# Optimization experiments

Hardware: AMD Instinct MI355X
Metric: run time of the kernel (lower is better)

Reference implementation:

```python
import jax, jax.numpy as jnp
import numpy as np

N, T, I, H = 256, 256, 512, 512

def setup_inputs() -> dict:
    key = jax.random.key(0)
    ks = jax.random.split(key, 9)
    s = 1.0 / np.sqrt(H)  # torch GRUCell init scale
    x = jax.random.normal(ks[0], (N, T, I), jnp.float32)
    is_init = jax.random.bernoulli(ks[1], 0.05, (N, T))  # bool resets
    hx = jax.random.normal(ks[2], (N, T, H), jnp.float32)
    W_ih = jax.random.uniform(ks[3], (3 * H, I), jnp.float32, -s, s)
    W_hh = jax.random.uniform(ks[4], (3 * H, H), jnp.float32, -s, s)
    b_ih = jax.random.uniform(ks[5], (3 * H,), jnp.float32, -s, s)
    b_hh = jax.random.uniform(ks[6], (3 * H,), jnp.float32, -s, s)
    W_out = jax.random.uniform(ks[7], (H, H), jnp.float32, -s, s)
    b_out = jax.random.uniform(ks[8], (H,), jnp.float32, -s, s)
    return {"x": x, "hx": hx, "W_ih": W_ih, "W_hh": W_hh, "b_ih": b_ih,
            "b_hh": b_hh, "W_out": W_out, "b_out": b_out, "is_init": is_init}

def _gru_forward(x, hx, W_ih, W_hh, b_ih, b_hh, W_out, b_out, is_init):
    # recurrent_mode branch; learnable_init=False -> reset to zeros
    mask = is_init[..., None]                         # [N,T,1] bool
    h0 = jnp.where(mask[:, 0], 0.0, hx[:, 0])        # [N,H]
    # precompute input-to-hidden gates for all steps: [N,T,3H]
    xi = jnp.einsum('nti,gi->ntg', x, W_ih) + b_ih

    def step(h, inp):
        xi_t, m_t = inp                              # [N,3H], [N,1]
        h = jnp.where(m_t, 0.0, h)                   # per-step init masking
        hh = h @ W_hh.T + b_hh                       # [N,3H]
        xr, xz, xn = jnp.split(xi_t, 3, axis=-1)
        hr, hz, hn = jnp.split(hh, 3, axis=-1)
        r = jax.nn.sigmoid(xr + hr)
        z = jax.nn.sigmoid(xz + hz)
        n = jnp.tanh(xn + r * hn)
        h_new = (1.0 - z) * n + z * h
        return h_new, h_new

    hT, hs = jax.lax.scan(step, h0,
                          (xi.transpose(1, 0, 2), mask.transpose(1, 0, 2)))
    hs = hs.transpose(1, 0, 2)                       # [N,T,H]
    output = hs @ W_out.T + b_out                    # LazyLinear projection
    hx_out = jnp.broadcast_to(hT[:, None, :], (hT.shape[0], T, hT.shape[1]))
    return output, hx_out

def reference(x, hx, W_ih, W_hh, b_ih, b_hh, W_out, b_out, is_init):
    return _gru_forward(x, hx, W_ih, W_hh, b_ih, b_hh, W_out, b_out, is_init)
```

## Files before the change

kernel.cpp:

```cpp
#include <hip/hip_runtime.h>

#define NB 256
#define TT 256
#define II 512
#define HH 512
#define GG 1536

typedef unsigned short ushort_t;
typedef unsigned int uint_t;
typedef unsigned long long ull_t;
typedef __attribute__((ext_vector_type(8))) short short8;
typedef __attribute__((ext_vector_type(4))) float f32x4;

typedef __attribute__((address_space(3))) void lds_void;
typedef const __attribute__((address_space(1))) void glb_void;

__device__ __forceinline__ ushort_t f2bf(float f) {
  union { float f; unsigned int u; } x; x.f = f;
  unsigned int r = x.u + 0x7FFFu + ((x.u >> 16) & 1u);
  return (ushort_t)(r >> 16);
}
__device__ __forceinline__ float bf2f(ushort_t b) {
  union { unsigned int u; float f; } x; x.u = ((unsigned int)b) << 16;
  return x.f;
}
__device__ __forceinline__ float sigmoidf_(float x) {
  return __fdividef(1.0f, 1.0f + __expf(-x));
}
__device__ __forceinline__ float tanhf_(float x) {
  float t = __expf(2.0f * x);
  return 1.0f - __fdividef(2.0f, t + 1.0f);
}
__device__ __forceinline__ short8 pack8(float4 a, float4 b) {
  short8 r;
  r[0] = (short)f2bf(a.x); r[1] = (short)f2bf(a.y);
  r[2] = (short)f2bf(a.z); r[3] = (short)f2bf(a.w);
  r[4] = (short)f2bf(b.x); r[5] = (short)f2bf(b.y);
  r[6] = (short)f2bf(b.z); r[7] = (short)f2bf(b.w);
  return r;
}

__global__ void mask_detect_kernel(const unsigned char* __restrict__ src,
                                   unsigned char* __restrict__ mask8) {
  __shared__ int fByte, fOdd;
  const int tid = threadIdx.x;
  if (tid == 0) { fByte = 0; fOdd = 0; }
  __syncthreads();
  const uint_t* w = (const uint_t*)src;
  int ab = 0, ao = 0;
  for (int i = tid; i < NB * TT; i += blockDim.x) {
    if ((i & 3) == 1 && src[i]) ab = 1;
    if (i < 16384 && (i & 1) == 1 && w[i]) ao = 1;
  }
  if (ab) fByte = 1;
  if (ao) fOdd = 1;
  __syncthreads();
  const int isByte = fByte, isW32 = fOdd;
  for (int i = tid; i < NB * TT; i += blockDim.x) {
    unsigned char m;
    if (isByte)      m = src[i] ? 1 : 0;
    else if (isW32)  m = w[i] ? 1 : 0;
    else             m = w[2 * i] ? 1 : 0;
    mask8[i] = m;
  }
}

__global__ void cvt_f2bf(const float* __restrict__ src, ushort_t* __restrict__ dst,
                         int n4) {
  int stride = gridDim.x * blockDim.x;
  for (int i = blockIdx.x * blockDim.x + threadIdx.x; i < n4; i += stride) {
    const float4 v = reinterpret_cast<const float4*>(src)[i];
    ushort4 o;
    o.x = f2bf(v.x); o.y = f2bf(v.y); o.z = f2bf(v.z); o.w = f2bf(v.w);
    reinterpret_cast<ushort4*>(dst)[i] = o;
  }
}

__global__ void pack_whh(const float* __restrict__ W, ushort_t* __restrict__ out) {
  int idx = blockIdx.x * blockDim.x + threadIdx.x;
  if (idx >= 96 * 16 * 64) return;
  int l = idx & 63;
  int tk = idx >> 6;
  int tile = tk >> 4, kk = tk & 15;
  int row = tile * 16 + (l & 15);
  int k = kk * 32 + (l >> 4) * 8;
  const float* s = W + (size_t)row * HH + k;
  short8 v;
#pragma unroll
  for (int e = 0; e < 8; ++e) v[e] = (short)f2bf(s[e]);
  *reinterpret_cast<short8*>(out + (size_t)idx * 8) = v;
}

template <int AF32, int CF32>
__global__ __launch_bounds__(256) void gemm_bt(
    const void* __restrict__ Av, const ushort_t* __restrict__ B,
    const float* __restrict__ bias, void* __restrict__ Cv, int NC) {
  __shared__ ushort_t As[128 * 32];
  __shared__ ushort_t Bs[128 * 32];
  const int tid = threadIdx.x;
  const int lane = tid & 63;
  const int w = tid >> 6;
  const int wr = w >> 1, wc = w & 1;
  const int c15 = lane & 15, l4 = lane >> 4;
  const int mbase = blockIdx.x * 128;
  const int nbase = blockIdx.y * 128;

  const int rs = tid >> 2;
  const int kb = (tid & 3) * 8;

  f32x4 acc[4][4] = {};

  const float4* Bg = reinterpret_cast<const float4*>(B);
  auto bIdx = [&](int c, int kt) {
    return ((size_t)(nbase + rs + 64 * c) * 512 + kt * 32 + kb) >> 3;
  };
  float4 rb0 = Bg[bIdx(0, 0)], rb1 = Bg[bIdx(1, 0)];

  const float4* Agf = reinterpret_cast<const float4*>(Av);
  auto aEl = [&](int c, int kt) {
    return (size_t)(mbase + rs + 64 * c) * 512 + kt * 32 + kb;
  };
  float4 a0a, a0b, a1a, a1b;
  float4 h0, h1;
  if constexpr (AF32) {
    a0a = Agf[aEl(0, 0) >> 2]; a0b = Agf[(aEl(0, 0) >> 2) + 1];
    a1a = Agf[aEl(1, 0) >> 2]; a1b = Agf[(aEl(1, 0) >> 2) + 1];
  } else {
    h0 = Agf[aEl(0, 0) >> 3];
    h1 = Agf[aEl(1, 0) >> 3];
  }

  for (int kt = 0; kt < 16; ++kt) {
    __syncthreads();
    if constexpr (AF32) {
      *reinterpret_cast<short8*>(&As[(size_t)tid * 8]) = pack8(a0a, a0b);
      *reinterpret_cast<short8*>(&As[(size_t)(tid + 256) * 8]) = pack8(a1a, a1b);
    } else {
      reinterpret_cast<float4*>(As)[tid] = h0;
      reinterpret_cast<float4*>(As)[tid + 256] = h1;
    }
    reinterpret_cast<float4*>(Bs)[tid] = rb0;
    reinterpret_cast<float4*>(Bs)[tid + 256] = rb1;
    if (kt < 15) {
      if constexpr (AF32) {
        a0a = Agf[aEl(0, kt + 1) >> 2]; a0b = Agf[(aEl(0, kt + 1) >> 2) + 1];
        a1a = Agf[aEl(1, kt + 1) >> 2]; a1b = Agf[(aEl(1, kt + 1) >> 2) + 1];
      } else {
        h0 = Agf[aEl(0, kt + 1) >> 3];
        h1 = Agf[aEl(1, kt + 1) >> 3];
      }
      rb0 = Bg[bIdx(0, kt + 1)]; rb1 = Bg[bIdx(1, kt + 1)];
    }
    __syncthreads();
    short8 af[4], bq[4];
#pragma unroll
    for (int m = 0; m < 4; ++m)
      af[m] = *reinterpret_cast<const short8*>(&As[(wr * 64 + m * 16 + c15) * 32 + l4 * 8]);
#pragma unroll
    for (int n = 0; n < 4; ++n)
      bq[n] = *reinterpret_cast<const short8*>(&Bs[(wc * 64 + n * 16 + c15) * 32 + l4 * 8]);
#pragma unroll
    for (int m = 0; m < 4; ++m)
#pragma unroll
      for (int n = 0; n < 4; ++n)
        acc[m][n] = __builtin_amdgcn_mfma_f32_16x16x32_bf16(af[m], bq[n], acc[m][n], 0, 0, 0);
  }

#pragma unroll
  for (int n = 0; n < 4; ++n) {
    const int col = nbase + wc * 64 + n * 16 + c15;
    const float bv = bias[col];
#pragma unroll
    for (int m = 0; m < 4; ++m) {
      const int row = mbase + wr * 64 + m * 16 + l4 * 4;
#pragma unroll
      for (int q = 0; q < 4; ++q) {
        const float v = acc[m][n][q] + bv;
        if constexpr (CF32)
          reinterpret_cast<float*>(Cv)[(size_t)(row + q) * NC + col] = v;
        else
          reinterpret_cast<ushort_t*>(Cv)[(size_t)(row + q) * NC + col] = f2bf(v);
      }
    }
  }
}

__global__ __launch_bounds__(256, 1) void gru_rec(
    const ushort_t* __restrict__ xi, const ushort_t* __restrict__ Wpk,
    const float* __restrict__ hx, const float* __restrict__ bhh,
    const unsigned char* __restrict__ mask8,
    ushort_t* __restrict__ hs, float* __restrict__ hT,
    char* __restrict__ xch) {
  extern __shared__ ushort_t smem[];
  const int HAF_U = 65536, XIL_U = 73728, HST_U = 79872;

  const int tid = threadIdx.x;
  const int lane = tid & 63;
  const int w = tid >> 6;
  const int c15 = lane & 15, l4 = lane >> 4;
  const int bid = blockIdx.x;
  const int a = bid & 7;
  const int b = bid >> 3;
  const int n0 = b * 16;

  const int jl = w * 16 + c15;
  const int jfull = a * 64 + jl;
  const float br = bhh[jfull], bz = bhh[512 + jfull], bn = bhh[1024 + jfull];

#pragma unroll
  for (int g = 0; g < 2; ++g)
#pragma unroll
    for (int kk = 0; kk < 16; ++kk)
      __builtin_amdgcn_global_load_lds(
          (glb_void*)(Wpk + ((size_t)((g * 32 + a * 4 + w) * 16 + kk)) * 512 + lane * 8),
          (lds_void*)(smem + w * 16384 + (g * 16 + kk) * 512 + lane * 8), 16, 0, 0);

  const int wb2 = ((2 * 32 + a * 4 + w) * 16) * 512 + lane * 8;
  short8 wn[16];
#pragma unroll
  for (int kk = 0; kk < 16; ++kk)
    wn[kk] = *(const short8*)(Wpk + wb2 + kk * 512);

  size_t xg0, xg1 = 0;
  {
    int c = tid, s = c / 24, r = c % 24, g = r >> 3, p = r & 7;
    xg0 = ((size_t)(n0 + s) * TT) * GG + g * 512 + a * 64 + p * 8;
    if (tid < 128) {
      c = tid + 256; s = c / 24; r = c % 24; g = r >> 3; p = r & 7;
      xg1 = ((size_t)(n0 + s) * TT) * GG + g * 512 + a * 64 + p * 8;
    }
  }
  const int xl0 = tid * 8, xl1 = (tid + 256) * 8;

  char* slot0 = xch + (size_t)(b * 2) * 32768;
  char* slot1 = xch + (size_t)(b * 2 + 1) * 32768;

  const int ps = tid >> 4, pj = tid & 15;
  const int pOff = (2 * a + (pj >> 3)) * 1024 +
                   (ps + 16 * ((pj >> 1) & 3)) * 16 + (pj & 1) * 8;
  const int pSrc = HST_U + ps * 72 + pj * 4;

  auto publish = [&](char* slot, uint_t tag) {
    const uint_t h0 = smem[pSrc], h1 = smem[pSrc + 1];
    const uint_t h2 = smem[pSrc + 2], h3 = smem[pSrc + 3];
    const ull_t w0 = ((ull_t)(h0 << 16 | tag)) | (((ull_t)(h1 << 16 | tag)) << 32);
    const ull_t w1 = ((ull_t)(h2 << 16 | tag)) | (((ull_t)(h3 << 16 | tag)) << 32);
    char* d = slot + (size_t)pOff * 2;
    __hip_atomic_store((ull_t*)d, w0, __ATOMIC_RELAXED, __HIP_MEMORY_SCOPE_AGENT);
    __hip_atomic_store((ull_t*)(d + 8), w1, __ATOMIC_RELAXED, __HIP_MEMORY_SCOPE_AGENT);
  };

  float h[4];
#pragma unroll
  for (int q = 0; q < 4; ++q) {
    const int s = l4 * 4 + q;
    const bool mk0 = mask8[(size_t)(n0 + s) * TT] != 0;
    const float v = mk0 ? 0.0f : hx[((size_t)(n0 + s) * TT) * HH + jfull];
    h[q] = v;
    smem[HST_U + s * 72 + jl] = f2bf(v);
  }
  __syncthreads();
  publish(slot0, 1u);

  for (int t = 0; t < TT; ++t) {
    ushort_t* xb = smem + XIL_U + (t & 1) * 3072;
    __builtin_amdgcn_global_load_lds((glb_void*)(xi + xg0 + (size_t)t * GG),
                                     (lds_void*)(xb + xl0), 16, 0, 0);
    if (tid < 128)
      __builtin_amdgcn_global_load_lds((glb_void*)(xi + xg1 + (size_t)t * GG),
                                       (lds_void*)(xb + xl1), 16, 0, 0);

    const char* src = (t & 1) ? slot1 : slot0;
    const uint_t tgt = (uint_t)(t + 1);
    ull_t v[16];
    bool ok;
    do {
      ok = true;
#pragma unroll
      for (int i = 0; i < 16; ++i)
        v[i] = __hip_atomic_load((const ull_t*)(src + ((size_t)(tid + i * 256)) * 8),
                                 __ATOMIC_RELAXED, __HIP_MEMORY_SCOPE_AGENT);
#pragma unroll
      for (int i = 0; i < 16; ++i)
        ok &= (((uint_t)v[i] & 0xFFFFu) == tgt) &&
              (((uint_t)(v[i] >> 32) & 0xFFFFu) == tgt);
    } while (!ok);
#pragma unroll
    for (int i = 0; i < 16; ++i) {
      const uint_t lo = (uint_t)(v[i] >> 16) & 0xFFFFu;
      const uint_t hi = (uint_t)(v[i] >> 48);
      *(uint_t*)((char*)smem + HAF_U * 2 + ((size_t)(tid + i * 256)) * 4) =
          lo | (hi << 16);
    }

    const bool domask = (t + 1 < TT);
    const int tn = domask ? (t + 1) : t;
    unsigned char mkv[4];
#pragma unroll
    for (int q = 0; q < 4; ++q)
      mkv[q] = mask8[(size_t)(n0 + l4 * 4 + q) * TT + tn];

    __syncthreads();

    short8 af[16];
#pragma unroll
    for (int kk = 0; kk < 16; ++kk)
      af[kk] = *(const short8*)((char*)smem + HAF_U * 2 + kk * 1024 + lane * 16);

    f32x4 a0 = {0.f, 0.f, 0.f, 0.f}, a1 = a0, a2 = a0;
#pragma unroll
    for (int kk = 0; kk < 16; ++kk) {
      const short8 w0 = *(const short8*)(smem + w * 16384 + kk * 512 + lane * 8);
      const short8 w1 = *(const short8*)(smem + w * 16384 + (16 + kk) * 512 + lane * 8);
      a0 = __builtin_amdgcn_mfma_f32_16x16x32_bf16(af[kk], w0, a0, 0, 0, 0);
      a1 = __builtin_amdgcn_mfma_f32_16x16x32_bf16(af[kk], w1, a1, 0, 0, 0);
      a2 = __builtin_amdgcn_mfma_f32_16x16x32_bf16(af[kk], wn[kk], a2, 0, 0, 0);
    }

#pragma unroll
    for (int q = 0; q < 4; ++q) {
      const int s = l4 * 4 + q;
      const float xr = bf2f(xb[s * 192 + jl]);
      const float xz = bf2f(xb[s * 192 + 64 + jl]);
      const float xn = bf2f(xb[s * 192 + 128 + jl]);
      const float rr = sigmoidf_(xr + a0[q] + br);
      const float zz = sigmoidf_(xz + a1[q] + bz);
      const float nn = tanhf_(xn + rr * (a2[q] + bn));
      const float hnew = (1.0f - zz) * nn + zz * h[q];
      __builtin_nontemporal_store(
          f2bf(hnew), &hs[((size_t)(n0 + s) * TT + t) * HH + jfull]);
      const float hp = (domask && mkv[q]) ? 0.0f : hnew;
      h[q] = hp;
      smem[HST_U + s * 72 + jl] = f2bf(hp);
    }
    __syncthreads();

    if (domask)
      publish(((t + 1) & 1) ? slot1 : slot0, (uint_t)(t + 2));
  }

#pragma unroll
  for (int q = 0; q < 4; ++q)
    hT[(size_t)(n0 + l4 * 4 + q) * HH + jfull] = h[q];
}

__global__ void bcast_hT(const float* __restrict__ hT, float* __restrict__ dst) {
  const float4* s = (const float4*)hT;
  float4* d = (float4*)dst;
  const int total = NB * TT * HH / 4;
  const int stride = gridDim.x * blockDim.x;
  for (int c = blockIdx.x * blockDim.x + threadIdx.x; c < total; c += stride) {
    int n = c >> 15;
    int j4 = c & 127;
    d[c] = s[(n << 7) | j4];
  }
}

extern "C" void kernel_launch(void* const* d_in, const int* in_sizes, int n_in,
                              void* d_out, int out_size, void* d_ws, size_t ws_size,
                              hipStream_t stream) {
  const float* x    = (const float*)d_in[0];
  const float* hx   = (const float*)d_in[1];
  const float* Wih  = (const float*)d_in[2];
  const float* Whh  = (const float*)d_in[3];
  const float* bih  = (const float*)d_in[4];
  const float* bhh  = (const float*)d_in[5];
  const float* Wout = (const float*)d_in[6];
  const float* bout = (const float*)d_in[7];
  const unsigned char* isinit = (const unsigned char*)d_in[8];

  char* ws = (char*)d_ws;
  ushort_t* xi    = (ushort_t*)(ws);
  ushort_t* wihb  = (ushort_t*)(ws + 201326592);
  ushort_t* whhp  = (ushort_t*)(ws + 202899456);
  ushort_t* woutb = (ushort_t*)(ws + 204472320);
  unsigned char* mask8 = (unsigned char*)(ws + 204996608);
  float*    hTbuf = (float*)(ws + 205062144);
  char*     xch   = (char*)(ws + 205602816);

  float* out1 = (float*)d_out;
  float* out2 = out1 + (size_t)NB * TT * HH;
  ushort_t* hsb = (ushort_t*)out2;

  hipMemsetAsync(xch, 0, 1 << 20, stream);
  mask_detect_kernel<<<1, 1024, 0, stream>>>(isinit, mask8);
  cvt_f2bf<<<768, 256, 0, stream>>>(Wih, wihb, GG * II / 4);
  cvt_f2bf<<<256, 256, 0, stream>>>(Wout, woutb, HH * HH / 4);
  pack_whh<<<384, 256, 0, stream>>>(Whh, whhp);

  dim3 g1(512, 12);
  gemm_bt<1, 0><<<g1, 256, 0, stream>>>((const void*)x, wihb, bih, (void*)xi, GG);

  gru_rec<<<128, 256, 162048, stream>>>(xi, whhp, hx, bhh, mask8, hsb, hTbuf,
                                        xch);

  dim3 g3(512, 4);
  gemm_bt<0, 1><<<g3, 256, 0, stream>>>((const void*)hsb, woutb, bout, (void*)out1, HH);

  bcast_hT<<<2048, 256, 0, stream>>>(hTbuf, out2);
}
```

Baseline: 1.349 ms.

## Publish hidden state directly from registers and skip polling own slice

The recurrent GRU kernel now has each lane pair shuffle its new bf16 hidden values and write them straight into a double-buffered LDS A-fragment and the global exchange slot. This removes the staging buffer and the second per-step __syncthreads. Each block no longer polls or copies its own slice of the exchange buffer. The r-gate weights move from LDS into registers alongside the n-gate weights, which shrinks LDS but adds register pressure. The hs stores are deferred until after publishing, so the cross-block critical path is shorter.

```diff
diff --git a/kernel.cpp b/kernel.cpp
--- a/kernel.cpp
+++ b/kernel.cpp
@@ -192,7 +192,7 @@
     ushort_t* __restrict__ hs, float* __restrict__ hT,
     char* __restrict__ xch) {
   extern __shared__ ushort_t smem[];
-  const int HAF_U = 65536, XIL_U = 73728, HST_U = 79872;
+  const int HAF_U = 32768, XIL_U = 49152;
 
   const int tid = threadIdx.x;
   const int lane = tid & 63;
@@ -208,18 +208,19 @@
   const float br = bhh[jfull], bz = bhh[512 + jfull], bn = bhh[1024 + jfull];
 
 #pragma unroll
-  for (int g = 0; g < 2; ++g)
-#pragma unroll
-    for (int kk = 0; kk < 16; ++kk)
-      __builtin_amdgcn_global_load_lds(
-          (glb_void*)(Wpk + ((size_t)((g * 32 + a * 4 + w) * 16 + kk)) * 512 + lane * 8),
-          (lds_void*)(smem + w * 16384 + (g * 16 + kk) * 512 + lane * 8), 16, 0, 0);
-
-  const int wb2 = ((2 * 32 + a * 4 + w) * 16) * 512 + lane * 8;
-  short8 wn[16];
-#pragma unroll
   for (int kk = 0; kk < 16; ++kk)
-    wn[kk] = *(const short8*)(Wpk + wb2 + kk * 512);
+    __builtin_amdgcn_global_load_lds(
+        (glb_void*)(Wpk + ((size_t)((32 + a * 4 + w) * 16 + kk)) * 512 + lane * 8),
+        (lds_void*)(smem + w * 8192 + kk * 512 + lane * 8), 16, 0, 0);
+
+  const int wbr = ((0 * 32 + a * 4 + w) * 16) * 512 + lane * 8;
+  const int wbn = ((2 * 32 + a * 4 + w) * 16) * 512 + lane * 8;
+  short8 wr_[16], wn_[16];
+#pragma unroll
+  for (int kk = 0; kk < 16; ++kk) {
+    wr_[kk] = *(const short8*)(Wpk + wbr + kk * 512);
+    wn_[kk] = *(const short8*)(Wpk + wbn + kk * 512);
+  }
 
   size_t xg0, xg1 = 0;
   {
@@ -235,32 +236,44 @@
   char* slot0 = xch + (size_t)(b * 2) * 32768;
   char* slot1 = xch + (size_t)(b * 2 + 1) * 32768;
 
-  const int ps = tid >> 4, pj = tid & 15;
-  const int pOff = (2 * a + (pj >> 3)) * 1024 +
-                   (ps + 16 * ((pj >> 1) & 3)) * 16 + (pj & 1) * 8;
-  const int pSrc = HST_U + ps * 72 + pj * 4;
-
-  auto publish = [&](char* slot, uint_t tag) {
-    const uint_t h0 = smem[pSrc], h1 = smem[pSrc + 1];
-    const uint_t h2 = smem[pSrc + 2], h3 = smem[pSrc + 3];
-    const ull_t w0 = ((ull_t)(h0 << 16 | tag)) | (((ull_t)(h1 << 16 | tag)) << 32);
-    const ull_t w1 = ((ull_t)(h2 << 16 | tag)) | (((ull_t)(h3 << 16 | tag)) << 32);
-    char* d = slot + (size_t)pOff * 2;
-    __hip_atomic_store((ull_t*)d, w0, __ATOMIC_RELAXED, __HIP_MEMORY_SCOPE_AGENT);
-    __hip_atomic_store((ull_t*)(d + 8), w1, __ATOMIC_RELAXED, __HIP_MEMORY_SCOPE_AGENT);
+  const bool evenlane = ((c15 & 1) == 0);
+  auto ubOff = [&](int s, int j) {
+    return (j >> 5) * 1024 + (s + 16 * ((j & 31) >> 3)) * 16 + (j & 7) * 2;
   };
 
+  auto pubfill = [&](char* slot, uint_t tag, int pp, const ushort_t* hb) {
+    const uint_t u01 = (uint_t)hb[0] | ((uint_t)hb[1] << 16);
+    const uint_t u23 = (uint_t)hb[2] | ((uint_t)hb[3] << 16);
+    const uint_t p01 = __shfl_xor(u01, 1);
+    const uint_t p23 = __shfl_xor(u23, 1);
+    if (evenlane) {
+      char* hafB = (char*)(smem + HAF_U + pp * 8192);
+#pragma unroll
+      for (int q = 0; q < 4; ++q) {
+        const int s = l4 * 4 + q;
+        const uint_t own = ((q < 2 ? u01 : u23) >> ((q & 1) * 16)) & 0xFFFFu;
+        const uint_t prt = ((q < 2 ? p01 : p23) >> ((q & 1) * 16)) & 0xFFFFu;
+        const int ub = ubOff(s, jfull);
+        *(uint_t*)(hafB + ub) = own | (prt << 16);
+        const ull_t wv = ((ull_t)((own << 16) | tag)) |
+                         (((ull_t)((prt << 16) | tag)) << 32);
+        __hip_atomic_store((ull_t*)(slot + (size_t)ub * 2), wv,
+                           __ATOMIC_RELAXED, __HIP_MEMORY_SCOPE_AGENT);
+      }
+    }
+  };
+
   float h[4];
+  ushort_t hb0[4];
 #pragma unroll
   for (int q = 0; q < 4; ++q) {
     const int s = l4 * 4 + q;
     const bool mk0 = mask8[(size_t)(n0 + s) * TT] != 0;
     const float v = mk0 ? 0.0f : hx[((size_t)(n0 + s) * TT) * HH + jfull];
     h[q] = v;
-    smem[HST_U + s * 72 + jl] = f2bf(v);
-  }
-  __syncthreads();
-  publish(slot0, 1u);
+    hb0[q] = f2bf(v);
+  }
+  pubfill(slot0, 1u, 0, hb0);
 
   for (int t = 0; t < TT; ++t) {
     ushort_t* xb = smem + XIL_U + (t & 1) * 3072;
@@ -282,16 +295,18 @@
                                  __ATOMIC_RELAXED, __HIP_MEMORY_SCOPE_AGENT);
 #pragma unroll
       for (int i = 0; i < 16; ++i)
-        ok &= (((uint_t)v[i] & 0xFFFFu) == tgt) &&
-              (((uint_t)(v[i] >> 32) & 0xFFFFu) == tgt);
+        if ((i >> 1) != a)
+          ok &= (((uint_t)v[i] & 0xFFFFu) == tgt) &&
+                (((uint_t)(v[i] >> 32) & 0xFFFFu) == tgt);
     } while (!ok);
-#pragma unroll
-    for (int i = 0; i < 16; ++i) {
-      const uint_t lo = (uint_t)(v[i] >> 16) & 0xFFFFu;
-      const uint_t hi = (uint_t)(v[i] >> 48);
-      *(uint_t*)((char*)smem + HAF_U * 2 + ((size_t)(tid + i * 256)) * 4) =
-          lo | (hi << 16);
-    }
+    char* hafB = (char*)(smem + HAF_U + (t & 1) * 8192);
+#pragma unroll
+    for (int i = 0; i < 16; ++i)
+      if ((i >> 1) != a) {
+        const uint_t lo = (uint_t)(v[i] >> 16) & 0xFFFFu;
+        const uint_t hi = (uint_t)(v[i] >> 48);
+        *(uint_t*)(hafB + ((size_t)(tid + i * 256)) * 4) = lo | (hi << 16);
+      }
 
     const bool domask = (t + 1 < TT);
     const int tn = domask ? (t + 1) : t;
@@ -305,18 +320,18 @@
     short8 af[16];
 #pragma unroll
     for (int kk = 0; kk < 16; ++kk)
-      af[kk] = *(const short8*)((char*)smem + HAF_U * 2 + kk * 1024 + lane * 16);
+      af[kk] = *(const short8*)(hafB + kk * 1024 + lane * 16);
 
     f32x4 a0 = {0.f, 0.f, 0.f, 0.f}, a1 = a0, a2 = a0;
 #pragma unroll
     for (int kk = 0; kk < 16; ++kk) {
-      const short8 w0 = *(const short8*)(smem + w * 16384 + kk * 512 + lane * 8);
-      const short8 w1 = *(const short8*)(smem + w * 16384 + (16 + kk) * 512 + lane * 8);
-      a0 = __builtin_amdgcn_mfma_f32_16x16x32_bf16(af[kk], w0, a0, 0, 0, 0);
-      a1 = __builtin_amdgcn_mfma_f32_16x16x32_bf16(af[kk], w1, a1, 0, 0, 0);
-      a2 = __builtin_amdgcn_mfma_f32_16x16x32_bf16(af[kk], wn[kk], a2, 0, 0, 0);
-    }
-
+      const short8 wz = *(const short8*)(smem + w * 8192 + kk * 512 + lane * 8);
+      a0 = __builtin_amdgcn_mfma_f32_16x16x32_bf16(af[kk], wr_[kk], a0, 0, 0, 0);
+      a1 = __builtin_amdgcn_mfma_f32_16x16x32_bf16(af[kk], wz, a1, 0, 0, 0);
+      a2 = __builtin_amdgcn_mfma_f32_16x16x32_bf16(af[kk], wn_[kk], a2, 0, 0, 0);
+    }
+
+    ushort_t hbp[4], hsv[4];
 #pragma unroll
     for (int q = 0; q < 4; ++q) {
       const int s = l4 * 4 + q;
@@ -327,16 +342,17 @@
       const float zz = sigmoidf_(xz + a1[q] + bz);
       const float nn = tanhf_(xn + rr * (a2[q] + bn));
       const float hnew = (1.0f - zz) * nn + zz * h[q];
-      __builtin_nontemporal_store(
-          f2bf(hnew), &hs[((size_t)(n0 + s) * TT + t) * HH + jfull]);
+      hsv[q] = f2bf(hnew);
       const float hp = (domask && mkv[q]) ? 0.0f : hnew;
       h[q] = hp;
-      smem[HST_U + s * 72 + jl] = f2bf(hp);
-    }
-    __syncthreads();
-
+      hbp[q] = f2bf(hp);
+    }
     if (domask)
-      publish(((t + 1) & 1) ? slot1 : slot0, (uint_t)(t + 2));
+      pubfill(((t + 1) & 1) ? slot1 : slot0, (uint_t)(t + 2), (t + 1) & 1, hbp);
+#pragma unroll
+    for (int q = 0; q < 4; ++q)
+      __builtin_nontemporal_store(
+          hsv[q], &hs[((size_t)(n0 + l4 * 4 + q) * TT + t) * HH + jfull]);
   }
 
 #pragma unroll
@@ -391,7 +407,7 @@
   dim3 g1(512, 12);
   gemm_bt<1, 0><<<g1, 256, 0, stream>>>((const void*)x, wihb, bih, (void*)xi, GG);
 
-  gru_rec<<<128, 256, 162048, stream>>>(xi, whhp, hx, bhh, mask8, hsb, hTbuf,
+  gru_rec<<<128, 256, 110592, stream>>>(xi, whhp, hx, bhh, mask8, hsb, hTbuf,
                                         xch);
 
   dim3 g3(512, 4);
```

Result: slower. 1.392 ms (+3.2%).
